# Performance work log

Measured on AMD Instinct MI355X. Metric: run time of the kernel, lower is better.

## Reference

```python
import jax, jax.numpy as jnp
import numpy as np

N, E, H, L, OUT, PDIM, NREL = 50000, 400000, 512, 4, 250, 2, 3
SLOPE = 0.2  # LeakyReLU negative slope


def leaky(x):
    return jnp.where(x > 0, x, SLOPE * x)


def seg_mean(msg, idx, n):
    # scatter-mean of per-edge messages onto destination nodes
    s = jax.ops.segment_sum(msg, idx, num_segments=n)
    c = jax.ops.segment_sum(jnp.ones((idx.shape[0], 1), msg.dtype), idx, num_segments=n)
    return s / jnp.maximum(c, 1.0)


def setup_inputs() -> dict:
    key = jax.random.key(0)
    ks = jax.random.split(key, 18)
    w = lambda k, shape: jax.random.normal(k, shape, dtype=jnp.float32) * 0.05
    return {
        "x_window": jax.random.normal(ks[0], (N, H), dtype=jnp.float32),
        "x_pos": jax.random.normal(ks[1], (N, PDIM), dtype=jnp.float32),
        "edge_near": jax.random.randint(ks[2], (2, E), 0, N),
        "edge_close": jax.random.randint(ks[3], (2, E), 0, N),
        "edge_sim": jax.random.randint(ks[4], (2, E), 0, N),
        "W_pre": w(ks[5], (H, H)),            # pretransform_win (no bias)
        "W_post": w(ks[6], (H, H)),           # post_plot_transform linear (no bias)
        "Wl": w(ks[7], (L, NREL, H, H)),      # SAGE neighbor transform per layer/relation
        "Wr": w(ks[8], (L, NREL, H, H)),      # SAGE self transform per layer/relation
        "Wpos": w(ks[9], (L, NREL, PDIM, H)), # edge_embed: relative-position embedding
        "Wg": w(ks[10], (L, H, H)),           # global vector injection per layer
        "seed": w(ks[11], (L, H)),            # GMPool_I seed query per layer
        "Wk": w(ks[12], (L, H, H)),
        "Wv": w(ks[13], (L, H, H)),
        "W_out": w(ks[14], (H, OUT)),
        "b_out": jnp.zeros((OUT,), jnp.float32),
    }


def reference(x_window, x_pos, edge_near, edge_close, edge_sim,
              W_pre, W_post, Wl, Wr, Wpos, Wg, seed, Wk, Wv, W_out, b_out):
    edges = (edge_near, edge_close, edge_sim)
    # pretransform + post_plot_transform: LeakyReLU -> Linear -> LeakyReLU
    x = leaky(leaky(x_window @ W_pre) @ W_post)
    inv_sqrt = np.float32(1.0 / np.sqrt(H))
    for l in range(L):
        # GMPool_I attention pooling over all nodes -> one global vector [H]
        attn = jax.nn.softmax(((x @ Wk[l]) @ seed[l]) * inv_sqrt)  # [N]
        g = attn @ (x @ Wv[l])                                      # [H]
        gterm = g @ Wg[l]                                           # [H]
        acc = jnp.zeros_like(x)
        for r in range(NREL):
            src, dst = edges[r][0], edges[r][1]
            # message = neighbor feature + relative-position edge embedding
            msg = x[src] + (x_pos[src] - x_pos[dst]) @ Wpos[l, r]   # [E,H]
            agg = seg_mean(msg, dst, N)                             # [N,H]
            acc = acc + agg @ Wl[l, r] + x @ Wr[l, r] + gterm
        x = leaky(acc / np.float32(NREL))  # HeteroConv aggr='mean' + LeakyReLU
    return x @ W_out + b_out
```

## Files before the change

kernel.cpp:

```cpp
#include <hip/hip_runtime.h>

#define NN 50000
#define EE 400000
#define HH 512
#define LL 4
#define OUTC 250
#define MP 50048
#define HH2 (HH*HH)
#define NPW 512
#define NBLK 49
#define INV_SQRT_H 0.044194173824159216f

typedef unsigned short u16;
typedef unsigned char u8;
typedef __attribute__((ext_vector_type(8))) unsigned short u16x8;
typedef __attribute__((ext_vector_type(8))) short s16x8;
typedef __attribute__((ext_vector_type(4))) float f32x4;
typedef __attribute__((ext_vector_type(2))) float f32x2;

__device__ __forceinline__ float b2f(u16 v) {
  union { unsigned u; float f; } c; c.u = ((unsigned)v) << 16; return c.f;
}
__device__ __forceinline__ u16 f2b(float f) {
  union { float f; unsigned u; } c; c.f = f;
  unsigned r = c.u + 0x7fffu + ((c.u >> 16) & 1u);
  return (u16)(r >> 16);
}
__device__ __forceinline__ float leakyf(float v) { return v > 0.f ? v : 0.2f * v; }

__device__ __forceinline__ void async16(const void* g, void* l) {
  __builtin_amdgcn_global_load_lds((const __attribute__((address_space(1))) void*)g,
                                   (__attribute__((address_space(3))) void*)l,
                                   16, 0, 0);
}

__global__ void k_hist(const int* __restrict__ e0, const int* __restrict__ e1,
                       const int* __restrict__ e2, int* __restrict__ cnt) {
  int r = blockIdx.y;
  const int* dst = (r == 0 ? e0 : r == 1 ? e1 : e2) + EE;
  int i = blockIdx.x * 256 + threadIdx.x;
  if (i < EE) atomicAdd(&cnt[r * NN + dst[i]], 1);
}

__global__ void k_scan1(const int* __restrict__ cnt, int* __restrict__ offs,
                        float* __restrict__ invc, int* __restrict__ bsum) {
  int r = blockIdx.y, b = blockIdx.x, t = threadIdx.x;
  int i = b * 1024 + t;
  int v = (i < NN) ? cnt[r * NN + i] : 0;
  __shared__ int sm[1024];
  sm[t] = v;
  __syncthreads();
#pragma unroll
  for (int d = 1; d < 1024; d <<= 1) {
    int u = (t >= d) ? sm[t - d] : 0;
    __syncthreads();
    sm[t] += u;
    __syncthreads();
  }
  if (i < NN) {
    offs[r * (NN + 1) + i] = sm[t] - v;
    invc[r * NN + i] = 1.f / (float)(v > 1 ? v : 1);
  }
  if (t == 1023) bsum[r * NBLK + b] = sm[t];
}

__global__ void k_scan2(int* __restrict__ bsum) {
  int t = threadIdx.x;
  int r = t >> 6, lane = t & 63;
  if (r >= 3) return;
  int orig = (lane < NBLK) ? bsum[r * NBLK + lane] : 0;
  int v = orig;
#pragma unroll
  for (int d = 1; d < 64; d <<= 1) {
    int u = __shfl_up(v, d);
    if (lane >= d) v += u;
  }
  if (lane < NBLK) bsum[r * NBLK + lane] = v - orig;
}

__global__ void k_scan3(const int* __restrict__ bsum, int* __restrict__ offs,
                        int* __restrict__ cursor) {
  int r = blockIdx.y, b = blockIdx.x, t = threadIdx.x;
  int i = b * 1024 + t;
  if (i < NN) {
    int v = offs[r * (NN + 1) + i] + bsum[r * NBLK + b];
    offs[r * (NN + 1) + i] = v;
    cursor[r * NN + i] = v;
  }
  if (b == 0 && t == 0) offs[r * (NN + 1) + NN] = EE;
}

__global__ void k_fill(const int* __restrict__ e0, const int* __restrict__ e1,
                       const int* __restrict__ e2,
                       int* __restrict__ cursor, int* __restrict__ csr) {
  int r = blockIdx.y;
  const int* ep = (r == 0 ? e0 : r == 1 ? e1 : e2);
  int i = blockIdx.x * 256 + threadIdx.x;
  if (i >= EE) return;
  int s = ep[i], d = ep[EE + i];
  int slot = atomicAdd(&cursor[r * NN + d], 1);
  csr[r * EE + slot] = s;
}

__global__ void k_pvec(const int* __restrict__ offs, const int* __restrict__ csr,
                       const float2* __restrict__ pos, float* __restrict__ P) {
  int r = blockIdx.y;
  int i = blockIdx.x * 256 + threadIdx.x;
  if (i >= NN) return;
  const int* o = offs + r * (NN + 1);
  const int* cs = csr + (size_t)r * EE;
  int b = o[i], e = o[i + 1];
  float sx = 0.f, sy = 0.f;
  for (int k = b; k < e; ++k) {
    float2 p = pos[cs[k]];
    sx += p.x; sy += p.y;
  }
  float2 pd = pos[i];
  float c = (float)(e - b);
  P[(size_t)r * NN * 2 + 2 * i]     = sx - c * pd.x;
  P[(size_t)r * NN * 2 + 2 * i + 1] = sy - c * pd.y;
}

__global__ void k_transT14(const float* __restrict__ Wl, const float* __restrict__ W_pre,
                           const float* __restrict__ W_post,
                           u16* __restrict__ wlT, u16* __restrict__ wpreT,
                           u16* __restrict__ wpostT) {
  __shared__ float sm[32][33];
  int z = blockIdx.z;
  const float* Wm; u16* WTm;
  if (z < 12)      { Wm = Wl + (size_t)z * HH2;  WTm = wlT + (size_t)z * HH2; }
  else if (z == 12){ Wm = W_pre;                  WTm = wpreT; }
  else             { Wm = W_post;                 WTm = wpostT; }
  int r0 = blockIdx.y * 32, c0 = blockIdx.x * 32;
  int tx = threadIdx.x, ty = threadIdx.y;
#pragma unroll
  for (int i = 0; i < 4; ++i)
    sm[ty + i * 8][tx] = Wm[(size_t)(r0 + ty + i * 8) * HH + c0 + tx];
  __syncthreads();
#pragma unroll
  for (int i = 0; i < 4; ++i)
    WTm[(size_t)(c0 + ty + i * 8) * HH + r0 + tx] = f2b(sm[tx][ty + i * 8]);
}

__global__ void k_sum3T(const float* __restrict__ Wr, u16* __restrict__ WT) {
  __shared__ float sm[32][33];
  int l = blockIdx.z;
  const float* W3 = Wr + (size_t)l * 3 * HH2;
  u16* WTm = WT + (size_t)l * HH2;
  int r0 = blockIdx.y * 32, c0 = blockIdx.x * 32;
  int tx = threadIdx.x, ty = threadIdx.y;
#pragma unroll
  for (int i = 0; i < 4; ++i) {
    size_t idx = (size_t)(r0 + ty + i * 8) * HH + c0 + tx;
    sm[ty + i * 8][tx] = W3[idx] + W3[HH2 + idx] + W3[2 * (size_t)HH2 + idx];
  }
  __syncthreads();
#pragma unroll
  for (int i = 0; i < 4; ++i)
    WTm[(size_t)(c0 + ty + i * 8) * HH + r0 + tx] = f2b(sm[tx][ty + i * 8]);
}

__global__ void k_transpose_pad(const float* __restrict__ W, u16* __restrict__ WT,
                                int rows, int cols, int tcols) {
  int idx = blockIdx.x * 256 + threadIdx.x;
  if (idx >= rows * tcols) return;
  int r = idx % rows, c = idx / rows;
  float v = (c < cols) ? W[(size_t)r * cols + c] : 0.f;
  WT[(size_t)c * rows + r] = f2b(v);
}

#define CVT_BLK ((NN * HH / 8 + 255) / 256)
__global__ void k_cvt_zero(const float* __restrict__ in, u16* __restrict__ out,
                           u16* a, u16* b, u16* c, u16* d, u16* e) {
  int blk = blockIdx.x;
  if (blk < CVT_BLK) {
    int i = blk * 256 + threadIdx.x;
    if (i >= NN * HH / 8) return;
    const float4 x = *(const float4*)(in + (size_t)i * 8);
    const float4 y = *(const float4*)(in + (size_t)i * 8 + 4);
    u16x8 o;
    o[0] = f2b(x.x); o[1] = f2b(x.y); o[2] = f2b(x.z); o[3] = f2b(x.w);
    o[4] = f2b(y.x); o[5] = f2b(y.y); o[6] = f2b(y.z); o[7] = f2b(y.w);
    *(u16x8*)(out + (size_t)i * 8) = o;
  } else {
    int i = (blk - CVT_BLK) * 256 + threadIdx.x;
    const int per = (MP - NN) * HH;
    if (i >= per * 5) return;
    int sel = i / per, rem = i - sel * per;
    u16* p = sel == 0 ? a : sel == 1 ? b : sel == 2 ? c : sel == 3 ? d : e;
    p[(size_t)NN * HH + rem] = 0;
  }
}

__global__ void k_kvec(const float* __restrict__ Wk, const float* __restrict__ seed,
                       float* __restrict__ kvec) {
  int l = blockIdx.x;
  const float* Wkl = Wk + (size_t)l * HH2;
  const float* sdl = seed + (size_t)l * HH;
  float* kv = kvec + (size_t)l * HH;
  int w = threadIdx.x >> 6, lane = threadIdx.x & 63;
  float sv[8];
#pragma unroll
  for (int i = 0; i < 8; ++i) sv[i] = sdl[lane * 8 + i];
  for (int row = w; row < HH; row += 8) {
    const float* p = Wkl + (size_t)row * HH + lane * 8;
    float d = 0.f;
#pragma unroll
    for (int i = 0; i < 8; ++i) d += p[i] * sv[i];
#pragma unroll
    for (int o = 32; o > 0; o >>= 1) d += __shfl_xor(d, o);
    if (lane == 0) kv[row] = d;
  }
}

__global__ void k_pool2g(const float* __restrict__ part, const float* __restrict__ Wv,
                         const float* __restrict__ Wg, float* __restrict__ gterm) {
  __shared__ float red[512];
  __shared__ float gv[HH];
  __shared__ float g[HH];
  int t = threadIdx.x;
  red[t] = part[(size_t)t * 514];
  __syncthreads();
  for (int s = 256; s > 0; s >>= 1) {
    if (t < s) red[t] = fmaxf(red[t], red[t + s]);
    __syncthreads();
  }
  float M = red[0];
  float s = 0.f, z = 0.f;
  for (int w = 0; w < NPW; ++w) {
    const float* p = part + (size_t)w * 514;
    float e = __expf(p[0] - M);
    z += e * p[1];
    s += e * p[2 + t];
  }
  gv[t] = s / z;
  __syncthreads();
  float a = 0.f;
  for (int i = 0; i < HH; ++i) a += gv[i] * Wv[(size_t)i * HH + t];
  g[t] = a;
  __syncthreads();
  float b = 0.f;
  for (int i = 0; i < HH; ++i) b += g[i] * Wg[(size_t)i * HH + t];
  gterm[t] = b;
}

__device__ __forceinline__ void acc_fp8x8(float* acc, uint2 v) {
  f32x2 a0 = __builtin_amdgcn_cvt_pk_f32_fp8(v.x, false);
  f32x2 a1 = __builtin_amdgcn_cvt_pk_f32_fp8(v.x, true);
  f32x2 a2 = __builtin_amdgcn_cvt_pk_f32_fp8(v.y, false);
  f32x2 a3 = __builtin_amdgcn_cvt_pk_f32_fp8(v.y, true);
  acc[0] += a0[0]; acc[1] += a0[1]; acc[2] += a1[0]; acc[3] += a1[1];
  acc[4] += a2[0]; acc[5] += a2[1]; acc[6] += a3[0]; acc[7] += a3[1];
}

__global__ void k_spmm_pool(const int* __restrict__ offs, const int* __restrict__ csr,
                            const float* __restrict__ invc, const float* __restrict__ P,
                            const float* __restrict__ wposL, const u16* __restrict__ x,
                            const u8* __restrict__ x8,
                            u16* __restrict__ agg, const float* __restrict__ kvec,
                            float* __restrict__ part) {
  int r = blockIdx.y;
  int lane = threadIdx.x & 63;
  if (r == 3) {
    if (blockIdx.x >= NPW / 4) return;
    int gw = (blockIdx.x * 256 + threadIdx.x) >> 6;
    float kl[8];
#pragma unroll
    for (int i = 0; i < 8; ++i) kl[i] = kvec[lane * 8 + i];
    float m = -1e30f, Z = 0.f;
    float acc[8] = {0, 0, 0, 0, 0, 0, 0, 0};
    for (int n = gw; n < NN; n += NPW) {
      u16x8 v = *(const u16x8*)(x + (size_t)n * HH + lane * 8);
      float xl[8], d = 0.f;
#pragma unroll
      for (int i = 0; i < 8; ++i) { xl[i] = b2f(v[i]); d += xl[i] * kl[i]; }
#pragma unroll
      for (int o = 32; o > 0; o >>= 1) d += __shfl_xor(d, o);
      d *= INV_SQRT_H;
      float mn = fmaxf(m, d);
      float c = __expf(m - mn), w = __expf(d - mn);
      Z = Z * c + w;
#pragma unroll
      for (int i = 0; i < 8; ++i) acc[i] = acc[i] * c + w * xl[i];
      m = mn;
    }
    float* p = part + (size_t)gw * 514;
#pragma unroll
    for (int i = 0; i < 8; ++i) p[2 + lane * 8 + i] = acc[i];
    if (lane == 0) { p[0] = m; p[1] = Z; }
    return;
  }
  int wv = __builtin_amdgcn_readfirstlane((int)(blockIdx.x * 256 + threadIdx.x) >> 6);
  if (wv >= NN) return;
  const int* o = offs + r * (NN + 1);
  const int* cs = csr + (size_t)r * EE;
  const float* wpos = wposL + (size_t)r * 2 * HH;
  int beg = o[wv], end = o[wv + 1];
  float acc[8] = {0, 0, 0, 0, 0, 0, 0, 0};
  int k = beg;
  for (; k + 7 < end; k += 8) {
    int s[8];
#pragma unroll
    for (int j = 0; j < 8; ++j) s[j] = cs[k + j];
    uint2 v[8];
#pragma unroll
    for (int j = 0; j < 8; ++j) v[j] = *(const uint2*)(x8 + (size_t)s[j] * HH + lane * 8);
#pragma unroll
    for (int j = 0; j < 8; ++j) acc_fp8x8(acc, v[j]);
  }
  for (; k + 3 < end; k += 4) {
    int s[4];
#pragma unroll
    for (int j = 0; j < 4; ++j) s[j] = cs[k + j];
    uint2 v[4];
#pragma unroll
    for (int j = 0; j < 4; ++j) v[j] = *(const uint2*)(x8 + (size_t)s[j] * HH + lane * 8);
#pragma unroll
    for (int j = 0; j < 4; ++j) acc_fp8x8(acc, v[j]);
  }
  for (; k < end; ++k) {
    uint2 v0 = *(const uint2*)(x8 + (size_t)cs[k] * HH + lane * 8);
    acc_fp8x8(acc, v0);
  }
  float px = P[(size_t)r * NN * 2 + 2 * wv], py = P[(size_t)r * NN * 2 + 2 * wv + 1];
  float ic = invc[(size_t)r * NN + wv];
  u16x8 out;
#pragma unroll
  for (int i = 0; i < 8; ++i) {
    float w0 = wpos[lane * 8 + i];
    float w1 = wpos[HH + lane * 8 + i];
    float v = (acc[i] + px * w0 + py * w1) * ic;
    out[i] = f2b(v);
  }
  __builtin_nontemporal_store(out, (u16x8*)(agg + ((size_t)r * MP + wv) * HH + lane * 8));
}

__global__ __launch_bounds__(256) void k_gemm(
    const u16* __restrict__ A0, const u16* __restrict__ A1,
    const u16* __restrict__ A2, const u16* __restrict__ A3,
    const u16* __restrict__ B0, const u16* __restrict__ B1,
    const u16* __restrict__ B2, const u16* __restrict__ B3,
    int nkt, int mode, float alpha, const float* __restrict__ gvec,
    u16* __restrict__ outB, u8* __restrict__ out8, float* __restrict__ outF,
    const float* __restrict__ bias, int M, int Nout, int G, int gx)
{
  __shared__ u16 lsA[128 * 64];
  __shared__ u16 lsB[128 * 64];
  const int tid = threadIdx.x;
  const int wave = tid >> 6, lane = tid & 63;
  const int wm = (wave >> 1) * 64, wn = (wave & 1) * 64;

  const int gid = blockIdx.x;
  const int q = G >> 3, rr = G & 7;
  const int xk = gid & 7, idx = gid >> 3;
  const int tl = xk * q + (xk < rr ? xk : rr) + idx;
  const int rowM0 = (tl / gx) * 128, colN0 = (tl % gx) * 128;

  f32x4 acc[4][4];
#pragma unroll
  for (int i = 0; i < 4; ++i)
#pragma unroll
    for (int j = 0; j < 4; ++j) acc[i][j] = (f32x4){0.f, 0.f, 0.f, 0.f};

  const int rowT = wave * 8 + (lane >> 3);
  const int c8 = lane & 7;
  int aoff[2][4], boff[2][4];
#pragma unroll
  for (int K0 = 0; K0 < 2; ++K0)
#pragma unroll
    for (int f = 0; f < 4; ++f) {
      const int cb = K0 * 4 + (lane >> 4);
      const int mm = wm + f * 16 + (lane & 15);
      const int nn = wn + f * 16 + (lane & 15);
      aoff[K0][f] = mm * 64 + ((cb ^ (mm & 7)) << 3);
      boff[K0][f] = nn * 64 + ((cb ^ (nn & 7)) << 3);
    }

  const int nkb = nkt >> 3;
  for (int kb = 0; kb < nkb; ++kb) {
    const u16* As = kb == 0 ? A0 : (kb == 1 ? A1 : (kb == 2 ? A2 : A3));
    const u16* Bs = kb == 0 ? B0 : (kb == 1 ? B1 : (kb == 2 ? B2 : B3));
    for (int k8 = 0; k8 < 8; ++k8) {
      const int koff = k8 * 64;
#pragma unroll
      for (int i = 0; i < 4; ++i) {
        const int r = i * 32 + rowT;
        const int scol = (c8 ^ (r & 7)) * 8;
        async16(As + (size_t)(rowM0 + r) * HH + koff + scol, &lsA[i * 2048 + wave * 512]);
        async16(Bs + (size_t)(colN0 + r) * HH + koff + scol, &lsB[i * 2048 + wave * 512]);
      }
      __syncthreads();
#pragma unroll
      for (int K0 = 0; K0 < 2; ++K0) {
        s16x8 af[4], bfr[4];
#pragma unroll
        for (int f = 0; f < 4; ++f) {
          af[f] = *(const s16x8*)&lsA[aoff[K0][f]];
          bfr[f] = *(const s16x8*)&lsB[boff[K0][f]];
        }
#pragma unroll
        for (int fm = 0; fm < 4; ++fm)
#pragma unroll
          for (int fn = 0; fn < 4; ++fn)
            acc[fm][fn] = __builtin_amdgcn_mfma_f32_16x16x32_bf16(af[fm], bfr[fn], acc[fm][fn], 0, 0, 0);
      }
      __syncthreads();
    }
  }

  u8* l8 = (u8*)lsA;
#pragma unroll
  for (int fm = 0; fm < 4; ++fm) {
#pragma unroll
    for (int fn = 0; fn < 4; ++fn) {
#pragma unroll
      for (int r = 0; r < 4; ++r) {
        const int rit = wm + fm * 16 + ((lane >> 4) << 2) + r;
        const int cit = wn + fn * 16 + (lane & 15);
        const int row = rowM0 + rit, col = colN0 + cit;
        float v = acc[fm][fn][r];
        if (mode == 0) {
          v = leakyf(v * alpha + (gvec ? gvec[col] : 0.f));
          outB[(size_t)row * HH + col] = f2b(v);
          if (out8) {
            int pk = __builtin_amdgcn_cvt_pk_fp8_f32(v, v, 0, false);
            l8[rit * 128 + cit] = (u8)pk;
          }
        } else {
          if (row < M && col < Nout)
            outF[(size_t)row * Nout + col] = v + (bias ? bias[col] : 0.f);
        }
      }
    }
  }
  if (mode == 0 && out8) {
    __syncthreads();
    const int rit = tid >> 1, hoff = (tid & 1) * 64;
    const uint4* src = (const uint4*)(l8 + rit * 128 + hoff);
    uint4 v0 = src[0], v1 = src[1], v2 = src[2], v3 = src[3];
    uint4* dst = (uint4*)(out8 + (size_t)(rowM0 + rit) * HH + colN0 + hoff);
    dst[0] = v0; dst[1] = v1; dst[2] = v2; dst[3] = v3;
  }
}

extern "C" void kernel_launch(void* const* d_in, const int* in_sizes, int n_in,
                              void* d_out, int out_size, void* d_ws, size_t ws_size,
                              hipStream_t stream) {
  (void)in_sizes; (void)n_in; (void)out_size;
  const float* x_window = (const float*)d_in[0];
  const float* x_pos    = (const float*)d_in[1];
  const int*   e0 = (const int*)d_in[2];
  const int*   e1 = (const int*)d_in[3];
  const int*   e2 = (const int*)d_in[4];
  const float* W_pre  = (const float*)d_in[5];
  const float* W_post = (const float*)d_in[6];
  const float* Wl   = (const float*)d_in[7];
  const float* Wr   = (const float*)d_in[8];
  const float* Wpos = (const float*)d_in[9];
  const float* Wg   = (const float*)d_in[10];
  const float* seed = (const float*)d_in[11];
  const float* Wk   = (const float*)d_in[12];
  const float* Wv   = (const float*)d_in[13];
  const float* W_out= (const float*)d_in[14];
  const float* b_out= (const float*)d_in[15];
  float* out = (float*)d_out;

  char* base = (char*)d_ws;
  size_t off = 0;
  auto alloc = [&](size_t bytes) -> char* {
    char* p = base + off;
    off += (bytes + 255) & ~(size_t)255;
    return p;
  };
  u16* x_a   = (u16*)alloc((size_t)MP * HH * 2);
  u16* x_b   = (u16*)alloc((size_t)MP * HH * 2);
  u16* agg0  = (u16*)alloc((size_t)MP * HH * 2);
  u16* agg1  = (u16*)alloc((size_t)MP * HH * 2);
  u16* agg2  = (u16*)alloc((size_t)MP * HH * 2);
  u8*  x8    = (u8*)alloc((size_t)MP * HH);
  u16* wlT   = (u16*)alloc((size_t)12 * HH2 * 2);
  u16* wrsT  = (u16*)alloc((size_t)4 * HH2 * 2);
  u16* wpreT = (u16*)alloc((size_t)HH2 * 2);
  u16* wpostT= (u16*)alloc((size_t)HH2 * 2);
  u16* woutT = (u16*)alloc((size_t)256 * HH * 2);
  int* offs  = (int*)alloc((size_t)3 * (NN + 1) * 4);
  int* curs  = (int*)alloc((size_t)3 * NN * 4);
  int* cnt   = (int*)alloc((size_t)3 * NN * 4);
  int* csr   = (int*)alloc((size_t)3 * EE * 4);
  float* invc = (float*)alloc((size_t)3 * NN * 4);
  float* P    = (float*)alloc((size_t)3 * NN * 2 * 4);
  float* kvec  = (float*)alloc((size_t)LL * HH * 4);
  float* gterm = (float*)alloc(HH * 4);
  int* bsum  = (int*)alloc((size_t)3 * NBLK * 4);
  float* part  = (float*)curs;
  if (off > ws_size) return;

  hipMemsetAsync(cnt, 0, (size_t)3 * NN * 4, stream);

  k_hist<<<dim3((EE + 255) / 256, 3), 256, 0, stream>>>(e0, e1, e2, cnt);
  k_scan1<<<dim3(NBLK, 3), 1024, 0, stream>>>(cnt, offs, invc, bsum);
  k_scan2<<<1, 256, 0, stream>>>(bsum);
  k_scan3<<<dim3(NBLK, 3), 1024, 0, stream>>>(bsum, offs, curs);
  k_fill<<<dim3((EE + 255) / 256, 3), 256, 0, stream>>>(e0, e1, e2, curs, csr);
  k_pvec<<<dim3((NN + 255) / 256, 3), 256, 0, stream>>>(offs, csr, (const float2*)x_pos, P);

  k_transT14<<<dim3(16, 16, 14), dim3(32, 8), 0, stream>>>(Wl, W_pre, W_post,
                                                           wlT, wpreT, wpostT);
  k_sum3T<<<dim3(16, 16, 4), dim3(32, 8), 0, stream>>>(Wr, wrsT);
  k_transpose_pad<<<(HH * 256) / 256, 256, 0, stream>>>(W_out, woutT, HH, OUTC, 256);
  k_kvec<<<LL, 512, 0, stream>>>(Wk, seed, kvec);

  const int padBlk = ((MP - NN) * HH * 5 + 255) / 256;
  k_cvt_zero<<<CVT_BLK + padBlk, 256, 0, stream>>>(x_window, x_b, x_a, x_b, agg0, agg1, agg2);

  const u16* nul = nullptr;
  const int G4 = 4 * (MP / 128), G2 = 2 * (MP / 128);
  k_gemm<<<G4, 256, 0, stream>>>(x_b, nul, nul, nul, wpreT, nul, nul, nul,
                                 8, 0, 1.f, nullptr, agg0, nullptr, nullptr, nullptr, NN, HH, G4, 4);
  k_gemm<<<G4, 256, 0, stream>>>(agg0, nul, nul, nul, wpostT, nul, nul, nul,
                                 8, 0, 1.f, nullptr, x_a, x8, nullptr, nullptr, NN, HH, G4, 4);

  u16* cur = x_a; u16* nxt = x_b;
  for (int l = 0; l < LL; ++l) {
    k_spmm_pool<<<dim3(NN / 4, 4), 256, 0, stream>>>(offs, csr, invc, P,
                                                     Wpos + (size_t)l * 3 * 2 * HH, cur, x8, agg0,
                                                     kvec + (size_t)l * HH, part);
    k_pool2g<<<1, 512, 0, stream>>>(part, Wv + (size_t)l * HH2, Wg + (size_t)l * HH2, gterm);
    k_gemm<<<G4, 256, 0, stream>>>(
        agg0, agg1, agg2, cur,
        wlT + (size_t)(l * 3 + 0) * HH2, wlT + (size_t)(l * 3 + 1) * HH2,
        wlT + (size_t)(l * 3 + 2) * HH2, wrsT + (size_t)l * HH2,
        32, 0, (1.f / 3.f), gterm, nxt, (l < LL - 1) ? x8 : nullptr, nullptr, nullptr, NN, HH, G4, 4);
    u16* t = cur; cur = nxt; nxt = t;
  }
  k_gemm<<<G2, 256, 0, stream>>>(cur, nul, nul, nul, woutT, nul, nul, nul,
                                 8, 1, 1.f, nullptr, nullptr, nullptr, out, b_out, NN, OUTC, G2, 2);
}
```

Before: 1.953 ms.

## Double-buffer GEMM LDS tiles and read fp8 features in attention pooling

The GEMM kernel now keeps two LDS tile buffers. It issues the async loads for the next k-tile before computing the current one, so each k-tile needs one barrier instead of two and load latency can overlap with MFMA work. This doubles the LDS footprint per block, which may reduce how many blocks fit on a CU. Separately, the pooling branch of the SpMM kernel reads the fp8 copy of the node features instead of the bf16 one, halving its bytes read at the cost of lower precision in the softmax pooling.

Measured after the change: 2.633 ms. +34.8%, slower.

```diff
diff --git a/kernel.cpp b/kernel.cpp
--- a/kernel.cpp
+++ b/kernel.cpp
@@ -10,6 +10,7 @@
 #define NPW 512
 #define NBLK 49
 #define INV_SQRT_H 0.044194173824159216f
+#define LBUF 16384
 
 typedef unsigned short u16;
 typedef unsigned char u8;
@@ -253,9 +254,18 @@
   acc[4] += a2[0]; acc[5] += a2[1]; acc[6] += a3[0]; acc[7] += a3[1];
 }
 
+__device__ __forceinline__ void unpack_fp8x8(float* xl, uint2 v) {
+  f32x2 a0 = __builtin_amdgcn_cvt_pk_f32_fp8(v.x, false);
+  f32x2 a1 = __builtin_amdgcn_cvt_pk_f32_fp8(v.x, true);
+  f32x2 a2 = __builtin_amdgcn_cvt_pk_f32_fp8(v.y, false);
+  f32x2 a3 = __builtin_amdgcn_cvt_pk_f32_fp8(v.y, true);
+  xl[0] = a0[0]; xl[1] = a0[1]; xl[2] = a1[0]; xl[3] = a1[1];
+  xl[4] = a2[0]; xl[5] = a2[1]; xl[6] = a3[0]; xl[7] = a3[1];
+}
+
 __global__ void k_spmm_pool(const int* __restrict__ offs, const int* __restrict__ csr,
                             const float* __restrict__ invc, const float* __restrict__ P,
-                            const float* __restrict__ wposL, const u16* __restrict__ x,
+                            const float* __restrict__ wposL,
                             const u8* __restrict__ x8,
                             u16* __restrict__ agg, const float* __restrict__ kvec,
                             float* __restrict__ part) {
@@ -270,10 +280,11 @@
     float m = -1e30f, Z = 0.f;
     float acc[8] = {0, 0, 0, 0, 0, 0, 0, 0};
     for (int n = gw; n < NN; n += NPW) {
-      u16x8 v = *(const u16x8*)(x + (size_t)n * HH + lane * 8);
+      uint2 v = *(const uint2*)(x8 + (size_t)n * HH + lane * 8);
       float xl[8], d = 0.f;
-#pragma unroll
-      for (int i = 0; i < 8; ++i) { xl[i] = b2f(v[i]); d += xl[i] * kl[i]; }
+      unpack_fp8x8(xl, v);
+#pragma unroll
+      for (int i = 0; i < 8; ++i) d += xl[i] * kl[i];
 #pragma unroll
       for (int o = 32; o > 0; o >>= 1) d += __shfl_xor(d, o);
       d *= INV_SQRT_H;
@@ -344,8 +355,7 @@
     u16* __restrict__ outB, u8* __restrict__ out8, float* __restrict__ outF,
     const float* __restrict__ bias, int M, int Nout, int G, int gx)
 {
-  __shared__ u16 lsA[128 * 64];
-  __shared__ u16 lsB[128 * 64];
+  __shared__ u16 lds[2 * LBUF];
   const int tid = threadIdx.x;
   const int wave = tid >> 6, lane = tid & 63;
   const int wm = (wave >> 1) * 64, wn = (wave & 1) * 64;
@@ -364,6 +374,23 @@
 
   const int rowT = wave * 8 + (lane >> 3);
   const int c8 = lane & 7;
+
+  auto STAGE = [&](int buf, int kt) {
+    const int kb = kt >> 3;
+    const int koff = (kt & 7) * 64;
+    const u16* As = kb == 0 ? A0 : (kb == 1 ? A1 : (kb == 2 ? A2 : A3));
+    const u16* Bs = kb == 0 ? B0 : (kb == 1 ? B1 : (kb == 2 ? B2 : B3));
+    u16* la = lds + buf * LBUF;
+    u16* lb = la + 8192;
+#pragma unroll
+    for (int i = 0; i < 4; ++i) {
+      const int r = i * 32 + rowT;
+      const int scol = (c8 ^ (r & 7)) * 8;
+      async16(As + (size_t)(rowM0 + r) * HH + koff + scol, la + i * 2048 + wave * 512);
+      async16(Bs + (size_t)(colN0 + r) * HH + koff + scol, lb + i * 2048 + wave * 512);
+    }
+  };
+
   int aoff[2][4], boff[2][4];
 #pragma unroll
   for (int K0 = 0; K0 < 2; ++K0)
@@ -376,39 +403,31 @@
       boff[K0][f] = nn * 64 + ((cb ^ (nn & 7)) << 3);
     }
 
-  const int nkb = nkt >> 3;
-  for (int kb = 0; kb < nkb; ++kb) {
-    const u16* As = kb == 0 ? A0 : (kb == 1 ? A1 : (kb == 2 ? A2 : A3));
-    const u16* Bs = kb == 0 ? B0 : (kb == 1 ? B1 : (kb == 2 ? B2 : B3));
-    for (int k8 = 0; k8 < 8; ++k8) {
-      const int koff = k8 * 64;
-#pragma unroll
-      for (int i = 0; i < 4; ++i) {
-        const int r = i * 32 + rowT;
-        const int scol = (c8 ^ (r & 7)) * 8;
-        async16(As + (size_t)(rowM0 + r) * HH + koff + scol, &lsA[i * 2048 + wave * 512]);
-        async16(Bs + (size_t)(colN0 + r) * HH + koff + scol, &lsB[i * 2048 + wave * 512]);
+  STAGE(0, 0);
+  __syncthreads();
+  for (int kt = 0; kt < nkt; ++kt) {
+    const int cur = kt & 1;
+    if (kt + 1 < nkt) STAGE(cur ^ 1, kt + 1);
+    const u16* la = lds + cur * LBUF;
+    const u16* lb = la + 8192;
+#pragma unroll
+    for (int K0 = 0; K0 < 2; ++K0) {
+      s16x8 af[4], bfr[4];
+#pragma unroll
+      for (int f = 0; f < 4; ++f) {
+        af[f] = *(const s16x8*)&la[aoff[K0][f]];
+        bfr[f] = *(const s16x8*)&lb[boff[K0][f]];
       }
-      __syncthreads();
-#pragma unroll
-      for (int K0 = 0; K0 < 2; ++K0) {
-        s16x8 af[4], bfr[4];
-#pragma unroll
-        for (int f = 0; f < 4; ++f) {
-          af[f] = *(const s16x8*)&lsA[aoff[K0][f]];
-          bfr[f] = *(const s16x8*)&lsB[boff[K0][f]];
-        }
-#pragma unroll
-        for (int fm = 0; fm < 4; ++fm)
-#pragma unroll
-          for (int fn = 0; fn < 4; ++fn)
-            acc[fm][fn] = __builtin_amdgcn_mfma_f32_16x16x32_bf16(af[fm], bfr[fn], acc[fm][fn], 0, 0, 0);
-      }
-      __syncthreads();
+#pragma unroll
+      for (int fm = 0; fm < 4; ++fm)
+#pragma unroll
+        for (int fn = 0; fn < 4; ++fn)
+          acc[fm][fn] = __builtin_amdgcn_mfma_f32_16x16x32_bf16(af[fm], bfr[fn], acc[fm][fn], 0, 0, 0);
     }
-  }
-
-  u8* l8 = (u8*)lsA;
+    __syncthreads();
+  }
+
+  u8* l8 = (u8*)lds;
 #pragma unroll
   for (int fm = 0; fm < 4; ++fm) {
 #pragma unroll
@@ -523,7 +542,7 @@
   u16* cur = x_a; u16* nxt = x_b;
   for (int l = 0; l < LL; ++l) {
     k_spmm_pool<<<dim3(NN / 4, 4), 256, 0, stream>>>(offs, csr, invc, P,
-                                                     Wpos + (size_t)l * 3 * 2 * HH, cur, x8, agg0,
+                                                     Wpos + (size_t)l * 3 * 2 * HH, x8, agg0,
                                                      kvec + (size_t)l * HH, part);
     k_pool2g<<<1, 512, 0, stream>>>(part, Wv + (size_t)l * HH2, Wg + (size_t)l * HH2, gterm);
     k_gemm<<<G4, 256, 0, stream>>>(
```
